# Kernel optimization log

Measured on AMD Instinct MI355X. Metric: run time of the kernel, lower is better.

The kernel has to match this reference:

```python
import jax, jax.numpy as jnp
import numpy as np

B, C, H, W = 16, 512, 64, 64
SCALE = 8
CQK = C // SCALE  # 64
EPS = 1e-6


def setup_inputs() -> dict:
    key = jax.random.key(0)
    ks = jax.random.split(key, 8)
    x = jax.random.normal(ks[0], (B, C, H, W), dtype=jnp.float32)
    # 1x1 conv weights stored as [out_ch, in_ch] (kernel_size=1)
    Wq = jax.random.normal(ks[1], (CQK, C), dtype=jnp.float32) * 0.02
    bq = jnp.zeros((CQK,), dtype=jnp.float32)
    Wk = jax.random.normal(ks[2], (CQK, C), dtype=jnp.float32) * 0.02
    bk = jnp.zeros((CQK,), dtype=jnp.float32)
    Wv = jax.random.normal(ks[3], (C, C), dtype=jnp.float32) * 0.02
    bv = jnp.zeros((C,), dtype=jnp.float32)
    # gamma is initialized to 0 in the module; use a nonzero value so the
    # output is non-trivial for kernel correctness checks.
    gamma = jax.random.normal(ks[4], (1,), dtype=jnp.float32)
    return {"x": x, "Wq": Wq, "bq": bq, "Wk": Wk, "bk": bk,
            "Wv": Wv, "bv": bv, "gamma": gamma}


def _l2norm_ch(t):
    # normalize over the channel axis (dim=-2), matching torch.norm(p=2, dim=-2)
    nrm = jnp.sqrt(jnp.sum(t * t, axis=-2, keepdims=True))
    return t / jnp.maximum(nrm, EPS)


def reference(x, Wq, bq, Wk, bk, Wv, bv, gamma):
    b, c, h, w = x.shape
    n = h * w
    xf = x.reshape(b, c, n)                                   # [B,C,N]
    # 1x1 convs == channel matmuls
    Q = jnp.einsum('oc,bcn->bon', Wq, xf) + bq[None, :, None]  # [B,cqk,N]
    K = jnp.einsum('oc,bcn->bon', Wk, xf) + bk[None, :, None]  # [B,cqk,N]
    V = jnp.einsum('oc,bcn->bon', Wv, xf) + bv[None, :, None]  # [B,C,N]
    Qn = _l2norm_ch(Q).transpose(0, 2, 1)                      # [B,N,cqk]
    Kn = _l2norm_ch(K)                                         # [B,cqk,N]
    # Taylor-softmax surrogate denominator
    denom = n + jnp.einsum('bnc,bc->bn', Qn, Kn.sum(axis=-1))  # [B,N]
    tailor = 1.0 / jnp.maximum(denom, 1e-6)                    # [B,N]
    # KtV accumulation: [B,cqk,C]
    matrix = jnp.einsum('bmn,bcn->bmc', Kn, V)
    value_sum = jnp.sum(V, axis=-1)[:, :, None]                # [B,C,1] -> broadcast
    matrix_sum = value_sum + jnp.einsum('bnm,bmc->bcn', Qn, matrix)  # [B,C,N]
    weight_value = matrix_sum * tailor[:, None, :]             # [B,C,N]
    out = gamma * weight_value.reshape(b, c, h, w)
    return jnp.nan_to_num(out, nan=0.0, posinf=1.0, neginf=-1.0)
```

## Files before the change

kernel.cpp:

```cpp
#include <hip/hip_runtime.h>


typedef __attribute__((ext_vector_type(8))) short short8_t;
typedef __attribute__((ext_vector_type(4))) float f32x4;

__device__ __forceinline__ unsigned short f2bf(float f) {
  union { float f; unsigned u; } v; v.f = f;
  unsigned r = v.u + 0x7FFFu + ((v.u >> 16) & 1u);
  return (unsigned short)(r >> 16);
}
__device__ __forceinline__ float bf2f(unsigned short h) {
  union { unsigned u; float f; } v; v.u = ((unsigned)h) << 16;
  return v.f;
}

#define MFMA(a, b, c) __builtin_amdgcn_mfma_f32_16x16x32_bf16((a), (b), (c), 0, 0, 0)

__global__ void k_prep(const float* __restrict__ Wq, const float* __restrict__ Wk,
                       unsigned short* __restrict__ Wqk) {
  int idx = blockIdx.x * 256 + threadIdx.x;
  int o = idx >> 9, c = idx & 511;
  float v = (o < 64) ? Wq[o * 512 + c] : Wk[(o - 64) * 512 + c];
  Wqk[idx] = f2bf(v);
}

__launch_bounds__(256, 2)
__global__ void k_qk(const float* __restrict__ x, const unsigned short* __restrict__ Wqk,
                     const float* __restrict__ bq, const float* __restrict__ bk,
                     unsigned short* __restrict__ QnT, unsigned short* __restrict__ KnG,
                     float* __restrict__ Ksum) {
  __shared__ __align__(16) unsigned char smem[77312];
  unsigned short* SAb[2] = {(unsigned short*)(smem + 0),
                            (unsigned short*)(smem + 18432)};
  unsigned short* SBb[2] = {(unsigned short*)(smem + 36864),
                            (unsigned short*)(smem + 55296)};
  unsigned short* EQ = (unsigned short*)(smem + 0);
  unsigned short* EK = (unsigned short*)(smem + 18432);
  float* ssq   = (float*)(smem + 73728);
  float* invq  = (float*)(smem + 75776);
  float* invk  = (float*)(smem + 76288);
  float* biasL = (float*)(smem + 76800);

  const int t = threadIdx.x;
  const int lane = t & 63, w = t >> 6;
  const int l15 = lane & 15, quad = lane >> 4;
  const int nt = blockIdx.x, b = blockIdx.y;
  const int n0 = nt * 128;
  const float* xb = x + (size_t)b * 512 * 4096;

  if (t < 128) biasL[t] = (t < 64) ? bq[t] : bk[t - 64];

  f32x4 acc[2][8];
#pragma unroll
  for (int i = 0; i < 2; ++i)
#pragma unroll
    for (int j = 0; j < 8; ++j) acc[i][j] = (f32x4){0.f, 0.f, 0.f, 0.f};

  const int nB = t & 127;
  const int cgB = t >> 7;
  const float* bsrc0 = xb + (size_t)(cgB * 32) * 4096 + n0 + nB;

  short8_t apre[4];
  float bpre[32];

#define QK_LOADA(kc_) do {                                                     \
    const int c0_ = (kc_) * 64;                                                \
    _Pragma("unroll")                                                          \
    for (int p = 0; p < 4; ++p) {                                              \
      int gid = t + p * 256; int o_ = gid >> 3, cg = gid & 7;                  \
      apre[p] = *(const short8_t*)(Wqk + o_ * 512 + c0_ + cg * 8);             \
    } } while (0)

#define QK_LOADB(kc_) do {                                                     \
    const float* s_ = bsrc0 + (size_t)(kc_) * 64 * 4096;                       \
    _Pragma("unroll")                                                          \
    for (int i = 0; i < 32; ++i) bpre[i] = s_[(size_t)i * 4096];               \
    } while (0)

#define QK_STORE(pb) do {                                                      \
    unsigned short* SAp = SAb[pb]; unsigned short* SBp = SBb[pb];              \
    _Pragma("unroll")                                                          \
    for (int p = 0; p < 4; ++p) {                                              \
      int gid = t + p * 256; int o_ = gid >> 3, cg = gid & 7;                  \
      *(short8_t*)(SAp + o_ * 72 + cg * 8) = apre[p];                          \
    }                                                                          \
    _Pragma("unroll")                                                          \
    for (int j = 0; j < 4; ++j) {                                              \
      short8_t v_;                                                             \
      _Pragma("unroll")                                                        \
      for (int e = 0; e < 8; ++e) v_[e] = (short)f2bf(bpre[j * 8 + e]);        \
      *(short8_t*)(SBp + nB * 72 + cgB * 32 + j * 8) = v_;                     \
    } } while (0)

#define QK_MM(pb) do {                                                         \
    const unsigned short* SAp = SAb[pb]; const unsigned short* SBp = SBb[pb];  \
    _Pragma("unroll")                                                          \
    for (int s = 0; s < 2; ++s) {                                              \
      short8_t a0 = *(const short8_t*)(SAp + (w * 32 + l15) * 72 + s * 32 + quad * 8);      \
      short8_t a1 = *(const short8_t*)(SAp + (w * 32 + 16 + l15) * 72 + s * 32 + quad * 8); \
      _Pragma("unroll")                                                        \
      for (int tc = 0; tc < 8; ++tc) {                                         \
        short8_t bf_ = *(const short8_t*)(SBp + (tc * 16 + l15) * 72 + s * 32 + quad * 8);  \
        acc[0][tc] = MFMA(a0, bf_, acc[0][tc]);                                \
        acc[1][tc] = MFMA(a1, bf_, acc[1][tc]);                                \
      } } } while (0)

  QK_LOADA(0); QK_LOADB(0);
#pragma unroll
  for (int kc = 0; kc < 8; ++kc) {
    const int pb = kc & 1;
    QK_STORE(pb);
    if (kc < 7) { QK_LOADA(kc + 1); QK_LOADB(kc + 1); }
    __syncthreads();
    QK_MM(pb);
  }
  __syncthreads();

#pragma unroll
  for (int trl = 0; trl < 2; ++trl)
#pragma unroll
    for (int reg = 0; reg < 4; ++reg) {
      int o = w * 32 + trl * 16 + quad * 4 + reg;
      float bias = biasL[o];
#pragma unroll
      for (int tc = 0; tc < 8; ++tc) acc[trl][tc][reg] += bias;
    }

#pragma unroll
  for (int tc = 0; tc < 8; ++tc) {
    float v = 0.f;
#pragma unroll
    for (int trl = 0; trl < 2; ++trl)
#pragma unroll
      for (int reg = 0; reg < 4; ++reg) {
        float q = acc[trl][tc][reg];
        v += q * q;
      }
    v += __shfl_xor(v, 16);
    v += __shfl_xor(v, 32);
    if (quad == 0) ssq[w * 128 + tc * 16 + l15] = v;
  }
  __syncthreads();
  if (t < 128) {
    float qs = ssq[t] + ssq[128 + t];
    float ks = ssq[256 + t] + ssq[384 + t];
    invq[t] = 1.0f / fmaxf(sqrtf(qs), 1e-6f);
    invk[t] = 1.0f / fmaxf(sqrtf(ks), 1e-6f);
  }
  __syncthreads();

  if (w < 2) {
#pragma unroll
    for (int trl = 0; trl < 2; ++trl)
#pragma unroll
      for (int tc = 0; tc < 8; ++tc) {
        int n = tc * 16 + l15;
        float inv = invq[n];
#pragma unroll
        for (int reg = 0; reg < 4; ++reg) {
          int o = w * 32 + trl * 16 + quad * 4 + reg;
          EQ[n * 72 + o] = f2bf(acc[trl][tc][reg] * inv);
        }
      }
  } else {
#pragma unroll
    for (int trl = 0; trl < 2; ++trl)
#pragma unroll
      for (int reg = 0; reg < 4; ++reg) {
        int m = (w - 2) * 32 + trl * 16 + quad * 4 + reg;
        float p = 0.f;
#pragma unroll
        for (int tc = 0; tc < 8; ++tc) {
          int n = tc * 16 + l15;
          float val = acc[trl][tc][reg] * invk[n];
          EK[m * 136 + n] = f2bf(val);
          p += val;
        }
        p += __shfl_xor(p, 1);
        p += __shfl_xor(p, 2);
        p += __shfl_xor(p, 4);
        p += __shfl_xor(p, 8);
        if (l15 == 0) atomicAdd(Ksum + b * 64 + m, p);
      }
  }
  __syncthreads();

  unsigned short* qdst = QnT + ((size_t)b * 4096 + n0) * 64;
#pragma unroll
  for (int p = 0; p < 4; ++p) {
    int idx = t + p * 256;
    int row = idx >> 3, seg = idx & 7;
    *(short8_t*)(qdst + row * 64 + seg * 8) = *(const short8_t*)(EQ + row * 72 + seg * 8);
  }
  unsigned short* kdst = KnG + (size_t)b * 64 * 4096 + n0;
#pragma unroll
  for (int p = 0; p < 4; ++p) {
    int idx = t + p * 256;
    int row = idx >> 4, seg = idx & 15;
    *(short8_t*)(kdst + (size_t)row * 4096 + seg * 8) =
        *(const short8_t*)(EK + row * 136 + seg * 8);
  }
#undef QK_LOADA
#undef QK_LOADB
#undef QK_STORE
#undef QK_MM
}

__launch_bounds__(256, 2)
__global__ void k_t(const float* __restrict__ x, const unsigned short* __restrict__ KnG,
                    float* __restrict__ Tpart, float* __restrict__ xsum) {
  __shared__ __align__(16) unsigned char smem[55296];
  unsigned short* SAb[2] = {(unsigned short*)(smem + 0),
                            (unsigned short*)(smem + 9216)};
  unsigned short* SBb[2] = {(unsigned short*)(smem + 18432),
                            (unsigned short*)(smem + 36864)};
  const int t = threadIdx.x;
  const int lane = t & 63, w = t >> 6;
  const int l15 = lane & 15, quad = lane >> 4;
  const int ns = blockIdx.x, ct = blockIdx.y, b = blockIdx.z;
  const int c0 = ct * 128;
  const float* xb = x + (size_t)b * 512 * 4096;
  const unsigned short* Knb = KnG + (size_t)b * 64 * 4096 + ns * 512;

  f32x4 acc[4][2];
#pragma unroll
  for (int i = 0; i < 4; ++i)
#pragma unroll
    for (int j = 0; j < 2; ++j) acc[i][j] = (f32x4){0.f, 0.f, 0.f, 0.f};

  const int row = t >> 1, half = t & 1;
  float xs = 0.f;
  const float* bbase = xb + (size_t)(c0 + row) * 4096 + ns * 512 + half * 32;

  short8_t apre[2];
  f32x4 bpre[8];

#define T_LOADA(ch_) do {                                                      \
    _Pragma("unroll")                                                          \
    for (int p = 0; p < 2; ++p) {                                              \
      int gid = t + p * 256; int m_ = gid >> 3, cg = gid & 7;                  \
      apre[p] = *(const short8_t*)(Knb + (size_t)m_ * 4096 + (ch_) * 64 + cg * 8); \
    } } while (0)

#define T_LOADB(ch_) do {                                                      \
    const float* s_ = bbase + (ch_) * 64;                                      \
    _Pragma("unroll")                                                          \
    for (int q = 0; q < 8; ++q) bpre[q] = *(const f32x4*)(s_ + q * 4);         \
    } while (0)

#define T_STORE(pb) do {                                                       \
    unsigned short* SAp = SAb[pb]; unsigned short* SBp = SBb[pb];              \
    _Pragma("unroll")                                                          \
    for (int p = 0; p < 2; ++p) {                                              \
      int gid = t + p * 256; int m_ = gid >> 3, cg = gid & 7;                  \
      *(short8_t*)(SAp + m_ * 72 + cg * 8) = apre[p];                          \
    }                                                                          \
    _Pragma("unroll")                                                          \
    for (int j = 0; j < 4; ++j) {                                              \
      short8_t v_;                                                             \
      _Pragma("unroll")                                                        \
      for (int e = 0; e < 4; ++e) {                                            \
        float f0 = bpre[j * 2][e], f1 = bpre[j * 2 + 1][e];                    \
        xs += f0 + f1;                                                         \
        v_[e] = (short)f2bf(f0); v_[4 + e] = (short)f2bf(f1);                  \
      }                                                                        \
      *(short8_t*)(SBp + row * 72 + half * 32 + j * 8) = v_;                   \
    } } while (0)

#define T_MM(pb) do {                                                          \
    const unsigned short* SAp = SAb[pb]; const unsigned short* SBp = SBb[pb];  \
    _Pragma("unroll")                                                          \
    for (int s = 0; s < 2; ++s) {                                              \
      short8_t af[4];                                                          \
      _Pragma("unroll")                                                        \
      for (int tm = 0; tm < 4; ++tm)                                           \
        af[tm] = *(const short8_t*)(SAp + (tm * 16 + l15) * 72 + s * 32 + quad * 8); \
      _Pragma("unroll")                                                        \
      for (int tcl = 0; tcl < 2; ++tcl) {                                      \
        short8_t bf_ = *(const short8_t*)(SBp + (w * 32 + tcl * 16 + l15) * 72 + s * 32 + quad * 8); \
        _Pragma("unroll")                                                      \
        for (int tm = 0; tm < 4; ++tm) acc[tm][tcl] = MFMA(af[tm], bf_, acc[tm][tcl]); \
      } } } while (0)

  T_LOADA(0); T_LOADB(0);
#pragma unroll
  for (int ch = 0; ch < 8; ++ch) {
    const int pb = ch & 1;
    T_STORE(pb);
    if (ch < 7) { T_LOADA(ch + 1); T_LOADB(ch + 1); }
    __syncthreads();
    T_MM(pb);
  }

  xs += __shfl_xor(xs, 1);
  if (half == 0) atomicAdd(xsum + b * 512 + c0 + row, xs);
  float* Tp = Tpart + ((size_t)(ns * 16 + b) * 64) * 512;
#pragma unroll
  for (int tm = 0; tm < 4; ++tm)
#pragma unroll
    for (int tcl = 0; tcl < 2; ++tcl)
#pragma unroll
      for (int reg = 0; reg < 4; ++reg) {
        int m = tm * 16 + quad * 4 + reg;
        int c = c0 + w * 32 + tcl * 16 + l15;
        Tp[(size_t)m * 512 + c] = acc[tm][tcl][reg];
      }
#undef T_LOADA
#undef T_LOADB
#undef T_STORE
#undef T_MM
}

__global__ void k_red(const float* __restrict__ Tpart, float* __restrict__ T) {
  size_t idx = (size_t)blockIdx.x * 256 + threadIdx.x;
  const f32x4* p = (const f32x4*)Tpart + idx;
  f32x4 s = p[0];
#pragma unroll
  for (int ns = 1; ns < 8; ++ns) s += p[(size_t)ns * 131072];
  ((f32x4*)T)[idx] = s;
}

__launch_bounds__(256, 2)
__global__ void k_mat(const float* __restrict__ T, const float* __restrict__ Wv,
                      const float* __restrict__ bv, const float* __restrict__ xsum,
                      const float* __restrict__ Ksum,
                      unsigned short* __restrict__ matT, float* __restrict__ Vsum) {
  __shared__ __align__(16) unsigned char smem[27136];
  float* ST = (float*)smem;
  float* SW = (float*)(smem + 17408);
  float* SV = (float*)(smem + 26112);
  const int t = threadIdx.x;
  const int cb = blockIdx.x, b = blockIdx.y;
  const int c0 = cb * 32;
  const int mp = t >> 3, cs = t & 7;
  f32x4 acc0 = (f32x4){0.f, 0.f, 0.f, 0.f};
  f32x4 acc1 = (f32x4){0.f, 0.f, 0.f, 0.f};

  for (int kc = 0; kc < 8; ++kc) {
    __syncthreads();
#pragma unroll
    for (int p = 0; p < 4; ++p) {
      int idx = t + p * 256;
      int row = idx >> 4, f4 = idx & 15;
      *(f32x4*)(ST + row * 68 + f4 * 4) =
          *(const f32x4*)(T + ((size_t)b * 64 + row) * 512 + kc * 64 + f4 * 4);
    }
#pragma unroll
    for (int p = 0; p < 2; ++p) {
      int idx = t + p * 256;
      int row = idx >> 4, f4 = idx & 15;
      *(f32x4*)(SW + row * 68 + f4 * 4) =
          *(const f32x4*)(Wv + (size_t)(c0 + row) * 512 + kc * 64 + f4 * 4);
    }
    __syncthreads();
#pragma unroll 4
    for (int kk = 0; kk < 64; kk += 4) {
      f32x4 t0 = *(const f32x4*)(ST + (2 * mp) * 68 + kk);
      f32x4 t1 = *(const f32x4*)(ST + (2 * mp + 1) * 68 + kk);
#pragma unroll
      for (int j = 0; j < 4; ++j) {
        f32x4 wv = *(const f32x4*)(SW + (cs + j * 8) * 68 + kk);
#pragma unroll
        for (int e = 0; e < 4; ++e) {
          acc0[j] = fmaf(t0[e], wv[e], acc0[j]);
          acc1[j] = fmaf(t1[e], wv[e], acc1[j]);
        }
      }
    }
  }
  float ks0 = Ksum[b * 64 + 2 * mp];
  float ks1 = Ksum[b * 64 + 2 * mp + 1];
#pragma unroll
  for (int j = 0; j < 4; ++j) {
    int c = c0 + cs + j * 8;
    float bvc = bv[c];
    unsigned lo = f2bf(acc0[j] + bvc * ks0);
    unsigned hi = f2bf(acc1[j] + bvc * ks1);
    *(unsigned*)(matT + ((size_t)b * 512 + c) * 64 + 2 * mp) = lo | (hi << 16);
  }
  {
    int cc = t >> 3, kp = t & 7;
    const float* wr = Wv + (size_t)(c0 + cc) * 512 + kp * 64;
    const float* xr = xsum + b * 512 + kp * 64;
    float s = 0.f;
    for (int i = 0; i < 64; ++i) s += wr[i] * xr[i];
    SV[cc * 8 + kp] = s;
  }
  __syncthreads();
  if (t < 32) {
    float s = 0.f;
#pragma unroll
    for (int i = 0; i < 8; ++i) s += SV[t * 8 + i];
    int c = c0 + t;
    Vsum[b * 512 + c] = s + 4096.0f * bv[c];
  }
}

__launch_bounds__(256, 2)
__global__ void k_out(const unsigned short* __restrict__ QnT,
                      const unsigned short* __restrict__ matT,
                      const float* __restrict__ Ksum, const float* __restrict__ Vsum,
                      const float* __restrict__ gamma, float* __restrict__ out) {
  __shared__ __align__(16) unsigned char smem[38144];
  unsigned short* SA = (unsigned short*)smem;
  unsigned short* SB = (unsigned short*)(smem + 18432);
  float* Ksl  = (float*)(smem + 36864);
  float* tail = (float*)(smem + 37120);
  float* vs   = (float*)(smem + 37632);
  const int t = threadIdx.x;
  const int lane = t & 63, w = t >> 6;
  const int l15 = lane & 15, quad = lane >> 4;
  const int nt = blockIdx.x, ct = blockIdx.y, b = blockIdx.z;
  const int n0 = nt * 128, c0 = ct * 128;

  const unsigned short* asrc = matT + ((size_t)b * 512 + c0) * 64;
  const unsigned short* bsrc = QnT + ((size_t)b * 4096 + n0) * 64;
#pragma unroll
  for (int p = 0; p < 4; ++p) {
    int idx = t + p * 256;
    int row = idx >> 3, seg = idx & 7;
    *(short8_t*)(SA + row * 72 + seg * 8) = *(const short8_t*)(asrc + row * 64 + seg * 8);
    *(short8_t*)(SB + row * 72 + seg * 8) = *(const short8_t*)(bsrc + row * 64 + seg * 8);
  }
  if (t < 64) Ksl[t] = Ksum[b * 64 + t];
  if (t >= 128) vs[t - 128] = Vsum[b * 512 + c0 + (t - 128)];
  __syncthreads();
  if (t < 128) {
    float d = 0.f;
#pragma unroll
    for (int mm = 0; mm < 64; ++mm) d += bf2f(SB[t * 72 + mm]) * Ksl[mm];
    tail[t] = 1.0f / fmaxf(4096.0f + d, 1e-6f);
  }

  f32x4 acc[2][8];
#pragma unroll
  for (int i = 0; i < 2; ++i)
#pragma unroll
    for (int j = 0; j < 8; ++j) acc[i][j] = (f32x4){0.f, 0.f, 0.f, 0.f};

#pragma unroll
  for (int s = 0; s < 2; ++s) {
    short8_t a0 = *(const short8_t*)(SA + (w * 32 + l15) * 72 + s * 32 + quad * 8);
    short8_t a1 = *(const short8_t*)(SA + (w * 32 + 16 + l15) * 72 + s * 32 + quad * 8);
#pragma unroll
    for (int tc = 0; tc < 8; ++tc) {
      short8_t bfr = *(const short8_t*)(SB + (tc * 16 + l15) * 72 + s * 32 + quad * 8);
      acc[0][tc] = MFMA(a0, bfr, acc[0][tc]);
      acc[1][tc] = MFMA(a1, bfr, acc[1][tc]);
    }
  }
  __syncthreads();
  const float g = gamma[0];
  float* ob = out + (size_t)b * 512 * 4096;
#pragma unroll
  for (int trl = 0; trl < 2; ++trl)
#pragma unroll
    for (int tc = 0; tc < 8; ++tc) {
      int n = tc * 16 + l15;
      float tl = tail[n] * g;
#pragma unroll
      for (int reg = 0; reg < 4; ++reg) {
        int cl = w * 32 + trl * 16 + quad * 4 + reg;
        float val = tl * (vs[cl] + acc[trl][tc][reg]);
        ob[(size_t)(c0 + cl) * 4096 + n0 + n] = val;
      }
    }
}

extern "C" void kernel_launch(void* const* d_in, const int* in_sizes, int n_in,
                              void* d_out, int out_size, void* d_ws, size_t ws_size,
                              hipStream_t stream) {
  const float* x     = (const float*)d_in[0];
  const float* Wq    = (const float*)d_in[1];
  const float* bq    = (const float*)d_in[2];
  const float* Wk    = (const float*)d_in[3];
  const float* bk    = (const float*)d_in[4];
  const float* Wv    = (const float*)d_in[5];
  const float* bv    = (const float*)d_in[6];
  const float* gamma = (const float*)d_in[7];
  float* out = (float*)d_out;
  char* ws = (char*)d_ws;

  float* Tpart = (float*)(ws + 0);
  float* T     = (float*)(ws + 16777216);
  float* xsum  = (float*)(ws + 18874368);
  float* Ksum  = (float*)(ws + 18907136);
  float* Vsum  = (float*)(ws + 18911232);
  unsigned short* Wqk  = (unsigned short*)(ws + 18944000);
  unsigned short* matT = (unsigned short*)(ws + 19075072);
  unsigned short* QnT  = (unsigned short*)(ws + 20123648);
  unsigned short* Kn   = (unsigned short*)(ws + 28512256);

  hipMemsetAsync(ws + 18874368, 0, 36864, stream);
  k_prep<<<256, 256, 0, stream>>>(Wq, Wk, Wqk);
  k_qk<<<dim3(32, 16), 256, 0, stream>>>(x, Wqk, bq, bk, QnT, Kn, Ksum);
  k_t<<<dim3(8, 4, 16), 256, 0, stream>>>(x, Kn, Tpart, xsum);
  k_red<<<512, 256, 0, stream>>>(Tpart, T);
  k_mat<<<dim3(16, 16), 256, 0, stream>>>(T, Wv, bv, xsum, Ksum, matT, Vsum);
  k_out<<<dim3(32, 4, 16), 256, 0, stream>>>(QnT, matT, Ksum, Vsum, gamma, out);
}
```

Baseline: 323.1 us.

## Fold Tpart reduction into k_mat, move tailor computation into k_t, drop memset

```diff
diff --git a/kernel.cpp b/kernel.cpp
--- a/kernel.cpp
+++ b/kernel.cpp
@@ -17,11 +17,14 @@
 #define MFMA(a, b, c) __builtin_amdgcn_mfma_f32_16x16x32_bf16((a), (b), (c), 0, 0, 0)
 
 __global__ void k_prep(const float* __restrict__ Wq, const float* __restrict__ Wk,
-                       unsigned short* __restrict__ Wqk) {
+                       unsigned short* __restrict__ Wqk,
+                       float* __restrict__ xsum, float* __restrict__ Ksum) {
   int idx = blockIdx.x * 256 + threadIdx.x;
   int o = idx >> 9, c = idx & 511;
   float v = (o < 64) ? Wq[o * 512 + c] : Wk[(o - 64) * 512 + c];
   Wqk[idx] = f2bf(v);
+  if (idx < 8192) xsum[idx] = 0.f;
+  if (idx < 1024) Ksum[idx] = 0.f;
 }
 
 __launch_bounds__(256, 2)
@@ -208,12 +211,15 @@
 
 __launch_bounds__(256, 2)
 __global__ void k_t(const float* __restrict__ x, const unsigned short* __restrict__ KnG,
-                    float* __restrict__ Tpart, float* __restrict__ xsum) {
-  __shared__ __align__(16) unsigned char smem[55296];
+                    float* __restrict__ Tpart, float* __restrict__ xsum,
+                    const unsigned short* __restrict__ QnT,
+                    const float* __restrict__ Ksum, float* __restrict__ tailor) {
+  __shared__ __align__(16) unsigned char smem[55552];
   unsigned short* SAb[2] = {(unsigned short*)(smem + 0),
                             (unsigned short*)(smem + 9216)};
   unsigned short* SBb[2] = {(unsigned short*)(smem + 18432),
                             (unsigned short*)(smem + 36864)};
+  float* Ksl = (float*)(smem + 55296);
   const int t = threadIdx.x;
   const int lane = t & 63, w = t >> 6;
   const int l15 = lane & 15, quad = lane >> 4;
@@ -221,6 +227,8 @@
   const int c0 = ct * 128;
   const float* xb = x + (size_t)b * 512 * 4096;
   const unsigned short* Knb = KnG + (size_t)b * 64 * 4096 + ns * 512;
+
+  if (t < 64) Ksl[t] = Ksum[b * 64 + t];
 
   f32x4 acc[4][2];
 #pragma unroll
@@ -289,6 +297,19 @@
     T_STORE(pb);
     if (ch < 7) { T_LOADA(ch + 1); T_LOADB(ch + 1); }
     __syncthreads();
+    if (ch == 0 && t < 128) {
+      int n = ns * 512 + ct * 128 + t;
+      const unsigned short* q = QnT + ((size_t)b * 4096 + n) * 64;
+      float d = 0.f;
+#pragma unroll
+      for (int s8 = 0; s8 < 8; ++s8) {
+        short8_t qv = *(const short8_t*)(q + s8 * 8);
+#pragma unroll
+        for (int e = 0; e < 8; ++e)
+          d += bf2f((unsigned short)qv[e]) * Ksl[s8 * 8 + e];
+      }
+      tailor[b * 4096 + n] = 1.0f / fmaxf(4096.0f + d, 1e-6f);
+    }
     T_MM(pb);
   }
 
@@ -311,17 +332,8 @@
 #undef T_MM
 }
 
-__global__ void k_red(const float* __restrict__ Tpart, float* __restrict__ T) {
-  size_t idx = (size_t)blockIdx.x * 256 + threadIdx.x;
-  const f32x4* p = (const f32x4*)Tpart + idx;
-  f32x4 s = p[0];
-#pragma unroll
-  for (int ns = 1; ns < 8; ++ns) s += p[(size_t)ns * 131072];
-  ((f32x4*)T)[idx] = s;
-}
-
 __launch_bounds__(256, 2)
-__global__ void k_mat(const float* __restrict__ T, const float* __restrict__ Wv,
+__global__ void k_mat(const float* __restrict__ Tpart, const float* __restrict__ Wv,
                       const float* __restrict__ bv, const float* __restrict__ xsum,
                       const float* __restrict__ Ksum,
                       unsigned short* __restrict__ matT, float* __restrict__ Vsum) {
@@ -342,8 +354,12 @@
     for (int p = 0; p < 4; ++p) {
       int idx = t + p * 256;
       int row = idx >> 4, f4 = idx & 15;
-      *(f32x4*)(ST + row * 68 + f4 * 4) =
-          *(const f32x4*)(T + ((size_t)b * 64 + row) * 512 + kc * 64 + f4 * 4);
+      const float* tp = Tpart + ((size_t)b * 64 + row) * 512 + kc * 64 + f4 * 4;
+      f32x4 s = *(const f32x4*)tp;
+#pragma unroll
+      for (int ns2 = 1; ns2 < 8; ++ns2)
+        s += *(const f32x4*)(tp + (size_t)ns2 * 524288);
+      *(f32x4*)(ST + row * 68 + f4 * 4) = s;
     }
 #pragma unroll
     for (int p = 0; p < 2; ++p) {
@@ -399,14 +415,13 @@
 __launch_bounds__(256, 2)
 __global__ void k_out(const unsigned short* __restrict__ QnT,
                       const unsigned short* __restrict__ matT,
-                      const float* __restrict__ Ksum, const float* __restrict__ Vsum,
+                      const float* __restrict__ tailG, const float* __restrict__ Vsum,
                       const float* __restrict__ gamma, float* __restrict__ out) {
-  __shared__ __align__(16) unsigned char smem[38144];
+  __shared__ __align__(16) unsigned char smem[37888];
   unsigned short* SA = (unsigned short*)smem;
   unsigned short* SB = (unsigned short*)(smem + 18432);
-  float* Ksl  = (float*)(smem + 36864);
-  float* tail = (float*)(smem + 37120);
-  float* vs   = (float*)(smem + 37632);
+  float* tail = (float*)(smem + 36864);
+  float* vs   = (float*)(smem + 37376);
   const int t = threadIdx.x;
   const int lane = t & 63, w = t >> 6;
   const int l15 = lane & 15, quad = lane >> 4;
@@ -422,15 +437,9 @@
     *(short8_t*)(SA + row * 72 + seg * 8) = *(const short8_t*)(asrc + row * 64 + seg * 8);
     *(short8_t*)(SB + row * 72 + seg * 8) = *(const short8_t*)(bsrc + row * 64 + seg * 8);
   }
-  if (t < 64) Ksl[t] = Ksum[b * 64 + t];
-  if (t >= 128) vs[t - 128] = Vsum[b * 512 + c0 + (t - 128)];
+  if (t < 128) tail[t] = tailG[b * 4096 + n0 + t];
+  else if (t < 256) vs[t - 128] = Vsum[b * 512 + c0 + (t - 128)];
   __syncthreads();
-  if (t < 128) {
-    float d = 0.f;
-#pragma unroll
-    for (int mm = 0; mm < 64; ++mm) d += bf2f(SB[t * 72 + mm]) * Ksl[mm];
-    tail[t] = 1.0f / fmaxf(4096.0f + d, 1e-6f);
-  }
 
   f32x4 acc[2][8];
 #pragma unroll
@@ -449,7 +458,6 @@
       acc[1][tc] = MFMA(a1, bfr, acc[1][tc]);
     }
   }
-  __syncthreads();
   const float g = gamma[0];
   float* ob = out + (size_t)b * 512 * 4096;
 #pragma unroll
@@ -481,21 +489,19 @@
   float* out = (float*)d_out;
   char* ws = (char*)d_ws;
 
-  float* Tpart = (float*)(ws + 0);
-  float* T     = (float*)(ws + 16777216);
-  float* xsum  = (float*)(ws + 18874368);
-  float* Ksum  = (float*)(ws + 18907136);
-  float* Vsum  = (float*)(ws + 18911232);
-  unsigned short* Wqk  = (unsigned short*)(ws + 18944000);
-  unsigned short* matT = (unsigned short*)(ws + 19075072);
-  unsigned short* QnT  = (unsigned short*)(ws + 20123648);
-  unsigned short* Kn   = (unsigned short*)(ws + 28512256);
-
-  hipMemsetAsync(ws + 18874368, 0, 36864, stream);
-  k_prep<<<256, 256, 0, stream>>>(Wq, Wk, Wqk);
+  float* Tpart  = (float*)(ws + 0);
+  float* xsum   = (float*)(ws + 16777216);
+  float* Ksum   = (float*)(ws + 16809984);
+  float* Vsum   = (float*)(ws + 16814080);
+  float* tailor = (float*)(ws + 16846848);
+  unsigned short* Wqk  = (unsigned short*)(ws + 17108992);
+  unsigned short* matT = (unsigned short*)(ws + 17240064);
+  unsigned short* QnT  = (unsigned short*)(ws + 18288640);
+  unsigned short* Kn   = (unsigned short*)(ws + 26677248);
+
+  k_prep<<<256, 256, 0, stream>>>(Wq, Wk, Wqk, xsum, Ksum);
   k_qk<<<dim3(32, 16), 256, 0, stream>>>(x, Wqk, bq, bk, QnT, Kn, Ksum);
-  k_t<<<dim3(8, 4, 16), 256, 0, stream>>>(x, Kn, Tpart, xsum);
-  k_red<<<512, 256, 0, stream>>>(Tpart, T);
-  k_mat<<<dim3(16, 16), 256, 0, stream>>>(T, Wv, bv, xsum, Ksum, matT, Vsum);
-  k_out<<<dim3(32, 4, 16), 256, 0, stream>>>(QnT, matT, Ksum, Vsum, gamma, out);
-}
+  k_t<<<dim3(8, 4, 16), 256, 0, stream>>>(x, Kn, Tpart, xsum, QnT, Ksum, tailor);
+  k_mat<<<dim3(16, 16), 256, 0, stream>>>(Tpart, Wv, bv, xsum, Ksum, matT, Vsum);
+  k_out<<<dim3(32, 4, 16), 256, 0, stream>>>(QnT, matT, tailor, Vsum, gamma, out);
+}
```

After: 324.9 us. About the same (+0.5%).
